# Performance work log

Hardware: AMD Instinct MI355X
Metric: run time of the kernel (lower is better)

## Reference

```python
import jax, jax.numpy as jnp
import numpy as np

N = 12288       # number of edge-triangle incidences
D_IN = 2        # input_dim
D_K = 8         # d_k
H1 = 32
H2 = 16
N_EDGES = 6144  # number of segments for scatter_softmax
N_TRI = 4096


def _layernorm(x, g, b, eps=1e-5):
    mu = jnp.mean(x, axis=-1, keepdims=True)
    var = jnp.mean((x - mu) ** 2, axis=-1, keepdims=True)
    return (x - mu) / jnp.sqrt(var + eps) * g + b


def _rmsnorm(x, w, eps=1e-6):
    rms = jnp.sqrt(jnp.mean(x ** 2, axis=-1, keepdims=True))
    return x / (rms + eps) * w


def setup_inputs() -> dict:
    key = jax.random.key(0)
    ks = jax.random.split(key, 16)

    def lin(k, out_d, in_d):
        k1, k2 = jax.random.split(k)
        bound = 1.0 / np.sqrt(in_d)
        W = jax.random.uniform(k1, (out_d, in_d), jnp.float32, -bound, bound)
        b = jax.random.uniform(k2, (out_d,), jnp.float32, -bound, bound)
        return W, b

    Wq, bq = lin(ks[0], D_K, D_IN)
    Wk, bk = lin(ks[1], D_K, D_IN)
    Wv, bv = lin(ks[2], D_K, D_IN)
    W1, b1 = lin(ks[3], H1, D_K)    # Linear(d_k, 32)
    Wr, br = lin(ks[4], H1, H1)     # ResBlock Linear(32, 32)
    W2, b2 = lin(ks[5], H2, H1)     # Linear(32, 16)
    W3, b3 = lin(ks[6], 1, H2)      # Linear(16, 1)

    return {
        "edge_features": jax.random.normal(ks[7], (N, D_IN), jnp.float32),
        "edge_ids_all": jax.random.randint(ks[8], (N,), 0, N_EDGES, jnp.int32),
        "triangle_ids_all": jax.random.randint(ks[9], (N,), 0, N_TRI, jnp.int32),
        "Wq": Wq, "bq": bq, "Wk": Wk, "bk": bk, "Wv": Wv, "bv": bv,
        "W1": W1, "b1": b1,
        "ln1_g": jnp.ones((H1,), jnp.float32), "ln1_b": jnp.zeros((H1,), jnp.float32),
        "rms_w": jnp.ones((H1,), jnp.float32),
        "Wr": Wr, "br": br,
        "ln2_g": jnp.ones((H1,), jnp.float32), "ln2_b": jnp.zeros((H1,), jnp.float32),
        "W2": W2, "b2": b2, "W3": W3, "b3": b3,
    }


def reference(edge_features, edge_ids_all, triangle_ids_all,
              Wq, bq, Wk, bk, Wv, bv,
              W1, b1, ln1_g, ln1_b, rms_w, Wr, br, ln2_g, ln2_b,
              W2, b2, W3, b3):
    q = edge_features @ Wq.T + bq          # [N, d_k]
    k = edge_features @ Wk.T + bk
    v = edge_features @ Wv.T + bv

    scores = (q @ k.T) / np.sqrt(D_K).astype(np.float32)   # [N, N]
    mask = triangle_ids_all[:, None] == triangle_ids_all[None, :]
    scores = jnp.where(mask, scores, -jnp.inf)
    attn = jax.nn.softmax(scores, axis=1)                   # row softmax
    attended = attn @ v                                     # [N, d_k]

    # attention_mlp
    h = _layernorm(attended @ W1.T + b1, ln1_g, ln1_b)
    h = jax.nn.gelu(h, approximate=False)
    h = h + jax.nn.relu(_rmsnorm(h, rms_w) @ Wr.T + br)     # ResBlock
    h = _layernorm(h, ln2_g, ln2_b)
    h = jax.nn.gelu(h @ W2.T + b2, approximate=False)
    logits = (h @ W3.T + b3)[:, 0]                          # [N]

    # scatter_softmax over edge_ids segments
    seg_max = jax.ops.segment_max(logits, edge_ids_all, num_segments=N_EDGES)
    seg_max = jnp.where(jnp.isfinite(seg_max), seg_max, 0.0)
    e = jnp.exp(logits - seg_max[edge_ids_all])
    seg_sum = jax.ops.segment_sum(e, edge_ids_all, num_segments=N_EDGES)
    weights = e / seg_sum[edge_ids_all]
    return weights
```

## Files before the change

kernel.cpp:

```cpp
#include <hip/hip_runtime.h>
#include <math.h>

#define N_INC   12288
#define N_EDGES 6144
#define N_TRI   4096
#define CAP_T   32
#define CAP_E   16

__device__ __forceinline__ float gelu_exact(float x) {
    return 0.5f * x * (1.0f + erff(x * 0.70710678118654752f));
}

__global__ void __launch_bounds__(256) k_qkv_fill(
    const float* __restrict__ ef, const int* __restrict__ eid, const int* __restrict__ tri,
    const float* __restrict__ Wk, const float* __restrict__ bk,
    const float* __restrict__ Wv, const float* __restrict__ bv,
    float* __restrict__ k, float* __restrict__ v,
    int* __restrict__ tri_cnt, int* __restrict__ tri_bkt,
    int* __restrict__ edge_cnt, int* __restrict__ edge_bkt)
{
    int i = blockIdx.x * 256 + threadIdx.x;
    float2 x = ((const float2*)ef)[i];
    float kk[8], vv[8];
#pragma unroll
    for (int d = 0; d < 8; d++) {
        kk[d] = fmaf(Wk[d*2], x.x, fmaf(Wk[d*2+1], x.y, bk[d]));
        vv[d] = fmaf(Wv[d*2], x.x, fmaf(Wv[d*2+1], x.y, bv[d]));
    }
    ((float4*)k)[i*2+0] = make_float4(kk[0],kk[1],kk[2],kk[3]);
    ((float4*)k)[i*2+1] = make_float4(kk[4],kk[5],kk[6],kk[7]);
    ((float4*)v)[i*2+0] = make_float4(vv[0],vv[1],vv[2],vv[3]);
    ((float4*)v)[i*2+1] = make_float4(vv[4],vv[5],vv[6],vv[7]);

    int t = tri[i];
    int s = atomicAdd(&tri_cnt[t], 1);
    if (s < CAP_T) tri_bkt[t * CAP_T + s] = i;
    int e = eid[i];
    s = atomicAdd(&edge_cnt[e], 1);
    if (s < CAP_E) edge_bkt[e * CAP_E + s] = i;
}

__global__ void __launch_bounds__(256) k_main(
    const float* __restrict__ ef,
    const float* __restrict__ kbuf, const float* __restrict__ vbuf,
    const int* __restrict__ tri, const int* __restrict__ tri_cnt, const int* __restrict__ tri_bkt,
    const float* __restrict__ Wq, const float* __restrict__ bq,
    const float* __restrict__ W1, const float* __restrict__ b1,
    const float* __restrict__ ln1g, const float* __restrict__ ln1b,
    const float* __restrict__ rmsw,
    const float* __restrict__ Wr, const float* __restrict__ br,
    const float* __restrict__ ln2g, const float* __restrict__ ln2b,
    const float* __restrict__ W2, const float* __restrict__ b2,
    const float* __restrict__ W3, const float* __restrict__ b3,
    float* __restrict__ logits)
{
    __shared__ float sW1[256], sb1[32], sg1[32], sB1[32], srw[32];
    __shared__ float sWr[1024], sbr[32], sg2[32], sB2[32];
    __shared__ float sW2[512], sb2[16], sW3[16];

    const int tid = threadIdx.x;
#define CP(dst, src, len) for (int x_ = tid; x_ < (len); x_ += 256) dst[x_] = src[x_];
    CP(sW1, W1, 256) CP(sb1, b1, 32) CP(sg1, ln1g, 32) CP(sB1, ln1b, 32) CP(srw, rmsw, 32)
    CP(sWr, Wr, 1024) CP(sbr, br, 32) CP(sg2, ln2g, 32) CP(sB2, ln2b, 32)
    CP(sW2, W2, 512) CP(sb2, b2, 16) CP(sW3, W3, 16)
#undef CP
    __syncthreads();

    const int g4 = blockIdx.x * 256 + tid;
    const int i  = g4 >> 2;
    const int lq = tid & 3;
    const int ob = lq * 8;

    float2 x = ((const float2*)ef)[i];
    float qi[8];
#pragma unroll
    for (int d = 0; d < 8; d++)
        qi[d] = fmaf(Wq[d*2], x.x, fmaf(Wq[d*2+1], x.y, bq[d]));

    int t = tri[i];
    int n = min(tri_cnt[t], CAP_T);
    const int* bkt = tri_bkt + t * CAP_T;

    float m = -1e30f, l = 0.f, acc[8];
#pragma unroll
    for (int d = 0; d < 8; d++) acc[d] = 0.f;

    for (int p0 = 0; p0 < n; p0 += 4) {
        int4 jv = *(const int4*)(bkt + p0);
        int jj[4] = { jv.x, jv.y, jv.z, jv.w };
        int j0 = jv.x;
        float sc[4], vl[4][8];
#pragma unroll
        for (int u = 0; u < 4; u++) {
            int j = (p0 + u < n) ? jj[u] : j0;
            float4 ka = ((const float4*)(kbuf + j*8))[0];
            float4 kb = ((const float4*)(kbuf + j*8))[1];
            float s8 = qi[0]*ka.x + qi[1]*ka.y + qi[2]*ka.z + qi[3]*ka.w
                     + qi[4]*kb.x + qi[5]*kb.y + qi[6]*kb.z + qi[7]*kb.w;
            sc[u] = (p0 + u < n) ? s8 * 0.35355339059327373f : -1e30f;
            float4 va = ((const float4*)(vbuf + j*8))[0];
            float4 vb = ((const float4*)(vbuf + j*8))[1];
            vl[u][0]=va.x; vl[u][1]=va.y; vl[u][2]=va.z; vl[u][3]=va.w;
            vl[u][4]=vb.x; vl[u][5]=vb.y; vl[u][6]=vb.z; vl[u][7]=vb.w;
        }
        float cm = fmaxf(fmaxf(sc[0], sc[1]), fmaxf(sc[2], sc[3]));
        float w0 = expf(sc[0]-cm), w1 = expf(sc[1]-cm);
        float w2 = expf(sc[2]-cm), w3 = expf(sc[3]-cm);
        float cl = w0 + w1 + w2 + w3;
        float nm = fmaxf(m, cm);
        float sa = expf(m - nm), sb = expf(cm - nm);
        l = l * sa + cl * sb;
#pragma unroll
        for (int d = 0; d < 8; d++)
            acc[d] = acc[d]*sa + sb*(w0*vl[0][d] + w1*vl[1][d] + w2*vl[2][d] + w3*vl[3][d]);
        m = nm;
    }
    float inv_l = 1.f / l;
    float att[8];
#pragma unroll
    for (int d = 0; d < 8; d++) att[d] = acc[d] * inv_l;

    float h[8];
#pragma unroll
    for (int oo = 0; oo < 8; oo++) {
        float a = sb1[ob+oo];
#pragma unroll
        for (int d = 0; d < 8; d++) a += sW1[(ob+oo)*8+d] * att[d];
        h[oo] = a;
    }
    {
        float s = 0.f;
#pragma unroll
        for (int oo = 0; oo < 8; oo++) s += h[oo];
        s += __shfl_xor(s, 1); s += __shfl_xor(s, 2);
        float mu = s * (1.f/32.f);
        float vs = 0.f;
#pragma unroll
        for (int oo = 0; oo < 8; oo++) { float d = h[oo]-mu; vs += d*d; }
        vs += __shfl_xor(vs, 1); vs += __shfl_xor(vs, 2);
        float is = 1.f / sqrtf(vs * (1.f/32.f) + 1e-5f);
#pragma unroll
        for (int oo = 0; oo < 8; oo++) h[oo] = (h[oo]-mu)*is*sg1[ob+oo] + sB1[ob+oo];
    }
#pragma unroll
    for (int oo = 0; oo < 8; oo++) h[oo] = gelu_exact(h[oo]);

    {
        float ss = 0.f;
#pragma unroll
        for (int oo = 0; oo < 8; oo++) ss += h[oo]*h[oo];
        ss += __shfl_xor(ss, 1); ss += __shfl_xor(ss, 2);
        float rms = sqrtf(ss * (1.f/32.f));
        float ir = 1.f / (rms + 1e-6f);
        float hn[8];
#pragma unroll
        for (int oo = 0; oo < 8; oo++) hn[oo] = h[oo]*ir*srw[ob+oo];
        float a[8];
#pragma unroll
        for (int oo = 0; oo < 8; oo++) a[oo] = sbr[ob+oo];
#pragma unroll
        for (int r = 0; r < 4; r++) {
            float g[8];
#pragma unroll
            for (int s8 = 0; s8 < 8; s8++) g[s8] = __shfl(hn[s8], r, 4);
#pragma unroll
            for (int oo = 0; oo < 8; oo++)
#pragma unroll
                for (int s8 = 0; s8 < 8; s8++)
                    a[oo] += sWr[(ob+oo)*32 + r*8 + s8] * g[s8];
        }
#pragma unroll
        for (int oo = 0; oo < 8; oo++) h[oo] += fmaxf(a[oo], 0.f);
    }
    {
        float s = 0.f;
#pragma unroll
        for (int oo = 0; oo < 8; oo++) s += h[oo];
        s += __shfl_xor(s, 1); s += __shfl_xor(s, 2);
        float mu = s * (1.f/32.f);
        float vs = 0.f;
#pragma unroll
        for (int oo = 0; oo < 8; oo++) { float d = h[oo]-mu; vs += d*d; }
        vs += __shfl_xor(vs, 1); vs += __shfl_xor(vs, 2);
        float is = 1.f / sqrtf(vs * (1.f/32.f) + 1e-5f);
#pragma unroll
        for (int oo = 0; oo < 8; oo++) h[oo] = (h[oo]-mu)*is*sg2[ob+oo] + sB2[ob+oo];
    }
    float a2[4];
#pragma unroll
    for (int j = 0; j < 4; j++) a2[j] = sb2[lq*4+j];
#pragma unroll
    for (int r = 0; r < 4; r++) {
        float g[8];
#pragma unroll
        for (int s8 = 0; s8 < 8; s8++) g[s8] = __shfl(h[s8], r, 4);
#pragma unroll
        for (int j = 0; j < 4; j++)
#pragma unroll
            for (int s8 = 0; s8 < 8; s8++)
                a2[j] += sW2[(lq*4+j)*32 + r*8 + s8] * g[s8];
    }
    float h2[4];
#pragma unroll
    for (int j = 0; j < 4; j++) h2[j] = gelu_exact(a2[j]);

    float lgp = 0.f;
#pragma unroll
    for (int j = 0; j < 4; j++) lgp += sW3[lq*4+j] * h2[j];
    lgp += __shfl_xor(lgp, 1); lgp += __shfl_xor(lgp, 2);
    if (lq == 0) logits[i] = lgp + b3[0];
}

__global__ void __launch_bounds__(256) k_edge_softmax(
    const float* __restrict__ logits, const int* __restrict__ edge_cnt,
    const int* __restrict__ edge_bkt, float* __restrict__ out)
{
    int e = blockIdx.x * 256 + threadIdx.x;
    int n = min(edge_cnt[e], CAP_E);
    if (n == 0) return;
    const int4* bp = (const int4*)(edge_bkt + e * CAP_E);
    int4 b0 = bp[0], b1 = bp[1], b2 = bp[2], b3 = bp[3];
    int idx[16] = { b0.x,b0.y,b0.z,b0.w, b1.x,b1.y,b1.z,b1.w,
                    b2.x,b2.y,b2.z,b2.w, b3.x,b3.y,b3.z,b3.w };
    int i0 = b0.x;
    float lg[16];
#pragma unroll
    for (int u = 0; u < 16; u++) {
        int j = (u < n) ? idx[u] : i0;
        float val = logits[j];
        lg[u] = (u < n) ? val : -1e30f;
    }
    float mx = -1e30f;
#pragma unroll
    for (int u = 0; u < 16; u++) mx = fmaxf(mx, lg[u]);
    float ex[16], sum = 0.f;
#pragma unroll
    for (int u = 0; u < 16; u++) { ex[u] = expf(lg[u] - mx); sum += ex[u]; }
    float inv = 1.f / sum;
#pragma unroll
    for (int u = 0; u < 16; u++) if (u < n) out[idx[u]] = ex[u] * inv;
}

extern "C" void kernel_launch(void* const* d_in, const int* in_sizes, int n_in,
                              void* d_out, int out_size, void* d_ws, size_t ws_size,
                              hipStream_t stream) {
    const float* ef   = (const float*)d_in[0];
    const int*   eid  = (const int*)d_in[1];
    const int*   tri  = (const int*)d_in[2];
    const float* Wq   = (const float*)d_in[3];  const float* bq = (const float*)d_in[4];
    const float* Wk   = (const float*)d_in[5];  const float* bk = (const float*)d_in[6];
    const float* Wv   = (const float*)d_in[7];  const float* bv = (const float*)d_in[8];
    const float* W1   = (const float*)d_in[9];  const float* b1 = (const float*)d_in[10];
    const float* ln1g = (const float*)d_in[11]; const float* ln1b = (const float*)d_in[12];
    const float* rmsw = (const float*)d_in[13];
    const float* Wr   = (const float*)d_in[14]; const float* br = (const float*)d_in[15];
    const float* ln2g = (const float*)d_in[16]; const float* ln2b = (const float*)d_in[17];
    const float* W2   = (const float*)d_in[18]; const float* b2 = (const float*)d_in[19];
    const float* W3   = (const float*)d_in[20]; const float* b3 = (const float*)d_in[21];

    float* ws   = (float*)d_ws;
    float* kbuf = ws;
    float* vbuf = kbuf + N_INC*8;
    float* logits = vbuf + N_INC*8;
    int* tri_cnt  = (int*)(logits + N_INC);
    int* edge_cnt = tri_cnt + N_TRI;
    int* tri_bkt  = edge_cnt + N_EDGES;
    int* edge_bkt = tri_bkt + N_TRI*CAP_T;

    hipMemsetAsync(tri_cnt, 0, (size_t)(N_TRI + N_EDGES) * sizeof(int), stream);

    k_qkv_fill<<<48, 256, 0, stream>>>(ef, eid, tri, Wk, bk, Wv, bv,
                                       kbuf, vbuf,
                                       tri_cnt, tri_bkt, edge_cnt, edge_bkt);
    k_main<<<192, 256, 0, stream>>>(ef, kbuf, vbuf, tri, tri_cnt, tri_bkt,
                                    Wq, bq, W1, b1, ln1g, ln1b, rmsw, Wr, br,
                                    ln2g, ln2b, W2, b2, W3, b3, logits);
    k_edge_softmax<<<24, 256, 0, stream>>>(logits, edge_cnt, edge_bkt, (float*)d_out);
}
```

Measured before the change: 116.9 us.

## Recompute K/V inline and fuse edge softmax into main kernel via last-arriver counter

Drops the precomputed K/V buffers: the main kernel now recomputes each neighbour's key and value from its 2-float input features using weights held in shared memory. The separate edge-softmax kernel is removed. Each incidence atomically increments a per-edge completion counter, and the last arriver for an edge computes that edge's segment softmax in place. This removes a kernel launch and the K/V global traffic, at the cost of extra ALU work, atomics with acquire-release ordering, and a second zeroed counter array.

```diff
diff --git a/kernel.cpp b/kernel.cpp
--- a/kernel.cpp
+++ b/kernel.cpp
@@ -6,32 +6,18 @@
 #define N_TRI   4096
 #define CAP_T   32
 #define CAP_E   16
+#define AGENT   __HIP_MEMORY_SCOPE_AGENT
 
 __device__ __forceinline__ float gelu_exact(float x) {
     return 0.5f * x * (1.0f + erff(x * 0.70710678118654752f));
 }
 
-__global__ void __launch_bounds__(256) k_qkv_fill(
-    const float* __restrict__ ef, const int* __restrict__ eid, const int* __restrict__ tri,
-    const float* __restrict__ Wk, const float* __restrict__ bk,
-    const float* __restrict__ Wv, const float* __restrict__ bv,
-    float* __restrict__ k, float* __restrict__ v,
+__global__ void __launch_bounds__(256) k_fill(
+    const int* __restrict__ eid, const int* __restrict__ tri,
     int* __restrict__ tri_cnt, int* __restrict__ tri_bkt,
     int* __restrict__ edge_cnt, int* __restrict__ edge_bkt)
 {
     int i = blockIdx.x * 256 + threadIdx.x;
-    float2 x = ((const float2*)ef)[i];
-    float kk[8], vv[8];
-#pragma unroll
-    for (int d = 0; d < 8; d++) {
-        kk[d] = fmaf(Wk[d*2], x.x, fmaf(Wk[d*2+1], x.y, bk[d]));
-        vv[d] = fmaf(Wv[d*2], x.x, fmaf(Wv[d*2+1], x.y, bv[d]));
-    }
-    ((float4*)k)[i*2+0] = make_float4(kk[0],kk[1],kk[2],kk[3]);
-    ((float4*)k)[i*2+1] = make_float4(kk[4],kk[5],kk[6],kk[7]);
-    ((float4*)v)[i*2+0] = make_float4(vv[0],vv[1],vv[2],vv[3]);
-    ((float4*)v)[i*2+1] = make_float4(vv[4],vv[5],vv[6],vv[7]);
-
     int t = tri[i];
     int s = atomicAdd(&tri_cnt[t], 1);
     if (s < CAP_T) tri_bkt[t * CAP_T + s] = i;
@@ -42,9 +28,13 @@
 
 __global__ void __launch_bounds__(256) k_main(
     const float* __restrict__ ef,
-    const float* __restrict__ kbuf, const float* __restrict__ vbuf,
-    const int* __restrict__ tri, const int* __restrict__ tri_cnt, const int* __restrict__ tri_bkt,
+    const int* __restrict__ eid, const int* __restrict__ tri,
+    const int* __restrict__ tri_cnt, const int* __restrict__ tri_bkt,
+    const int* __restrict__ edge_cnt, const int* __restrict__ edge_bkt,
+    int* __restrict__ edge_done,
     const float* __restrict__ Wq, const float* __restrict__ bq,
+    const float* __restrict__ Wk, const float* __restrict__ bk,
+    const float* __restrict__ Wv, const float* __restrict__ bv,
     const float* __restrict__ W1, const float* __restrict__ b1,
     const float* __restrict__ ln1g, const float* __restrict__ ln1b,
     const float* __restrict__ rmsw,
@@ -52,14 +42,16 @@
     const float* __restrict__ ln2g, const float* __restrict__ ln2b,
     const float* __restrict__ W2, const float* __restrict__ b2,
     const float* __restrict__ W3, const float* __restrict__ b3,
-    float* __restrict__ logits)
+    float* __restrict__ logits, float* __restrict__ out)
 {
+    __shared__ float sWq[16], sbq[8], sWk[16], sbk[8], sWv[16], sbv[8];
     __shared__ float sW1[256], sb1[32], sg1[32], sB1[32], srw[32];
     __shared__ float sWr[1024], sbr[32], sg2[32], sB2[32];
     __shared__ float sW2[512], sb2[16], sW3[16];
 
     const int tid = threadIdx.x;
 #define CP(dst, src, len) for (int x_ = tid; x_ < (len); x_ += 256) dst[x_] = src[x_];
+    CP(sWq, Wq, 16) CP(sbq, bq, 8) CP(sWk, Wk, 16) CP(sbk, bk, 8) CP(sWv, Wv, 16) CP(sbv, bv, 8)
     CP(sW1, W1, 256) CP(sb1, b1, 32) CP(sg1, ln1g, 32) CP(sB1, ln1b, 32) CP(srw, rmsw, 32)
     CP(sWr, Wr, 1024) CP(sbr, br, 32) CP(sg2, ln2g, 32) CP(sB2, ln2b, 32)
     CP(sW2, W2, 512) CP(sb2, b2, 16) CP(sW3, W3, 16)
@@ -75,7 +67,7 @@
     float qi[8];
 #pragma unroll
     for (int d = 0; d < 8; d++)
-        qi[d] = fmaf(Wq[d*2], x.x, fmaf(Wq[d*2+1], x.y, bq[d]));
+        qi[d] = fmaf(sWq[d*2], x.x, fmaf(sWq[d*2+1], x.y, sbq[d]));
 
     int t = tri[i];
     int n = min(tri_cnt[t], CAP_T);
@@ -93,15 +85,15 @@
 #pragma unroll
         for (int u = 0; u < 4; u++) {
             int j = (p0 + u < n) ? jj[u] : j0;
-            float4 ka = ((const float4*)(kbuf + j*8))[0];
-            float4 kb = ((const float4*)(kbuf + j*8))[1];
-            float s8 = qi[0]*ka.x + qi[1]*ka.y + qi[2]*ka.z + qi[3]*ka.w
-                     + qi[4]*kb.x + qi[5]*kb.y + qi[6]*kb.z + qi[7]*kb.w;
+            float2 xj = ((const float2*)ef)[j];
+            float s8 = 0.f;
+#pragma unroll
+            for (int d = 0; d < 8; d++) {
+                float kd = fmaf(sWk[d*2], xj.x, fmaf(sWk[d*2+1], xj.y, sbk[d]));
+                s8 = fmaf(qi[d], kd, s8);
+                vl[u][d] = fmaf(sWv[d*2], xj.x, fmaf(sWv[d*2+1], xj.y, sbv[d]));
+            }
             sc[u] = (p0 + u < n) ? s8 * 0.35355339059327373f : -1e30f;
-            float4 va = ((const float4*)(vbuf + j*8))[0];
-            float4 vb = ((const float4*)(vbuf + j*8))[1];
-            vl[u][0]=va.x; vl[u][1]=va.y; vl[u][2]=va.z; vl[u][3]=va.w;
-            vl[u][4]=vb.x; vl[u][5]=vb.y; vl[u][6]=vb.z; vl[u][7]=vb.w;
         }
         float cm = fmaxf(fmaxf(sc[0], sc[1]), fmaxf(sc[2], sc[3]));
         float w0 = expf(sc[0]-cm), w1 = expf(sc[1]-cm);
@@ -208,37 +200,44 @@
 #pragma unroll
     for (int j = 0; j < 4; j++) lgp += sW3[lq*4+j] * h2[j];
     lgp += __shfl_xor(lgp, 1); lgp += __shfl_xor(lgp, 2);
-    if (lq == 0) logits[i] = lgp + b3[0];
-}
-
-__global__ void __launch_bounds__(256) k_edge_softmax(
-    const float* __restrict__ logits, const int* __restrict__ edge_cnt,
-    const int* __restrict__ edge_bkt, float* __restrict__ out)
-{
-    int e = blockIdx.x * 256 + threadIdx.x;
-    int n = min(edge_cnt[e], CAP_E);
-    if (n == 0) return;
-    const int4* bp = (const int4*)(edge_bkt + e * CAP_E);
-    int4 b0 = bp[0], b1 = bp[1], b2 = bp[2], b3 = bp[3];
-    int idx[16] = { b0.x,b0.y,b0.z,b0.w, b1.x,b1.y,b1.z,b1.w,
-                    b2.x,b2.y,b2.z,b2.w, b3.x,b3.y,b3.z,b3.w };
-    int i0 = b0.x;
-    float lg[16];
-#pragma unroll
-    for (int u = 0; u < 16; u++) {
-        int j = (u < n) ? idx[u] : i0;
-        float val = logits[j];
-        lg[u] = (u < n) ? val : -1e30f;
-    }
-    float mx = -1e30f;
-#pragma unroll
-    for (int u = 0; u < 16; u++) mx = fmaxf(mx, lg[u]);
-    float ex[16], sum = 0.f;
-#pragma unroll
-    for (int u = 0; u < 16; u++) { ex[u] = expf(lg[u] - mx); sum += ex[u]; }
-    float inv = 1.f / sum;
-#pragma unroll
-    for (int u = 0; u < 16; u++) if (u < n) out[idx[u]] = ex[u] * inv;
+    float lg = lgp + b3[0];
+
+    int e = eid[i];
+    int ne = edge_cnt[e];
+    int old = 0;
+    if (lq == 0) {
+        __hip_atomic_store(&logits[i], lg, __ATOMIC_RELAXED, AGENT);
+        old = __hip_atomic_fetch_add(&edge_done[e], 1, __ATOMIC_ACQ_REL, AGENT);
+    }
+    old = __shfl(old, 0, 4);
+
+    if (old == ne - 1) {
+        int nn = min(ne, CAP_E);
+        const int* eb = edge_bkt + e * CAP_E;
+        int idx0 = eb[0];
+        int   midx[4];
+        float mlg[4];
+        float lmax = -1e30f;
+#pragma unroll
+        for (int u = 0; u < 4; u++) {
+            int mth = lq + u * 4;
+            int j = (mth < nn) ? eb[mth] : idx0;
+            midx[u] = j;
+            float val = __hip_atomic_load(&logits[j], __ATOMIC_RELAXED, AGENT);
+            mlg[u] = (mth < nn) ? val : -1e30f;
+            lmax = fmaxf(lmax, mlg[u]);
+        }
+        lmax = fmaxf(lmax, __shfl_xor(lmax, 1));
+        lmax = fmaxf(lmax, __shfl_xor(lmax, 2));
+        float ex[4], lsum = 0.f;
+#pragma unroll
+        for (int u = 0; u < 4; u++) { ex[u] = expf(mlg[u] - lmax); lsum += ex[u]; }
+        lsum += __shfl_xor(lsum, 1); lsum += __shfl_xor(lsum, 2);
+        float inv = 1.f / lsum;
+#pragma unroll
+        for (int u = 0; u < 4; u++)
+            if (lq + u * 4 < nn) out[midx[u]] = ex[u] * inv;
+    }
 }
 
 extern "C" void kernel_launch(void* const* d_in, const int* in_sizes, int n_in,
@@ -258,22 +257,20 @@
     const float* W2   = (const float*)d_in[18]; const float* b2 = (const float*)d_in[19];
     const float* W3   = (const float*)d_in[20]; const float* b3 = (const float*)d_in[21];
 
-    float* ws   = (float*)d_ws;
-    float* kbuf = ws;
-    float* vbuf = kbuf + N_INC*8;
-    float* logits = vbuf + N_INC*8;
-    int* tri_cnt  = (int*)(logits + N_INC);
-    int* edge_cnt = tri_cnt + N_TRI;
-    int* tri_bkt  = edge_cnt + N_EDGES;
-    int* edge_bkt = tri_bkt + N_TRI*CAP_T;
-
-    hipMemsetAsync(tri_cnt, 0, (size_t)(N_TRI + N_EDGES) * sizeof(int), stream);
-
-    k_qkv_fill<<<48, 256, 0, stream>>>(ef, eid, tri, Wk, bk, Wv, bv,
-                                       kbuf, vbuf,
-                                       tri_cnt, tri_bkt, edge_cnt, edge_bkt);
-    k_main<<<192, 256, 0, stream>>>(ef, kbuf, vbuf, tri, tri_cnt, tri_bkt,
-                                    Wq, bq, W1, b1, ln1g, ln1b, rmsw, Wr, br,
-                                    ln2g, ln2b, W2, b2, W3, b3, logits);
-    k_edge_softmax<<<24, 256, 0, stream>>>(logits, edge_cnt, edge_bkt, (float*)d_out);
-}
+    float* ws     = (float*)d_ws;
+    float* logits = ws;
+    int* tri_cnt   = (int*)(logits + N_INC);
+    int* edge_cnt  = tri_cnt + N_TRI;
+    int* edge_done = edge_cnt + N_EDGES;
+    int* tri_bkt   = edge_done + N_EDGES;
+    int* edge_bkt  = tri_bkt + N_TRI*CAP_T;
+
+    hipMemsetAsync(tri_cnt, 0, (size_t)(N_TRI + 2 * N_EDGES) * sizeof(int), stream);
+
+    k_fill<<<48, 256, 0, stream>>>(eid, tri, tri_cnt, tri_bkt, edge_cnt, edge_bkt);
+    k_main<<<192, 256, 0, stream>>>(ef, eid, tri, tri_cnt, tri_bkt, edge_cnt, edge_bkt,
+                                    edge_done,
+                                    Wq, bq, Wk, bk, Wv, bv,
+                                    W1, b1, ln1g, ln1b, rmsw, Wr, br, ln2g, ln2b,
+                                    W2, b2, W3, b3, logits, (float*)d_out);
+}
```

Result: slower. 127.0 us (+8.6%).
